# Performance work log

Measured on AMD Instinct MI355X. Metric: run time of the kernel, lower is better.

The kernel has to match this reference:

```python
import jax, jax.numpy as jnp
import numpy as np
from jax import lax

# HF MambaConfig defaults with vocab_size=2048, hidden_size=128
V, DM, NL, I, N, K, R = 2048, 128, 32, 256, 16, 4, 8  # vocab, d_model, layers, intermediate, ssm_state, conv_kernel, dt_rank
B, L = 8, 2048
EPS = 1e-5


def _rms(x, w):
    return x * lax.rsqrt(jnp.mean(x * x, axis=-1, keepdims=True) + EPS) * w


def _block(x, p):
    res = x
    h = _rms(x, p['norm_w'])
    hz = h @ p['in_proj_w'].T                            # (B,L,2I)
    hs, gate = hz[..., :I], hz[..., I:]
    # depthwise causal conv over time
    c = lax.conv_general_dilated(hs.transpose(0, 2, 1), p['conv_w'][:, None, :],
                                 (1,), [(K - 1, 0)],
                                 dimension_numbers=('NCH', 'OIH', 'NCH'),
                                 feature_group_count=I)
    hs = jax.nn.silu((c + p['conv_b'][None, :, None]).transpose(0, 2, 1))  # (B,L,I)
    xp = hs @ p['x_proj_w'].T                            # (B,L,R+2N)
    dt, Bm, Cm = xp[..., :R], xp[..., R:R + N], xp[..., R + N:]
    dt = jax.nn.softplus(dt @ p['dt_proj_w'].T + p['dt_proj_b'])           # (B,L,I)
    A = -jnp.exp(p['A_log'])                             # (I,N)
    dA = jnp.exp(dt[..., None] * A)                      # (B,L,I,N)
    dBu = dt[..., None] * Bm[:, :, None, :] * hs[..., None]               # (B,L,I,N)

    # selective scan: h_t = dA_t * h_{t-1} + dBu_t, via parallel associative scan
    def comb(e1, e2):
        a1, b1 = e1
        a2, b2 = e2
        return a2 * a1, a2 * b1 + b2

    _, hstates = lax.associative_scan(comb, (dA, dBu), axis=1)
    y = jnp.einsum('blin,bln->bli', hstates, Cm) + hs * p['D']
    y = y * jax.nn.silu(gate)
    return res + y @ p['out_proj_w'].T


def setup_inputs() -> dict:
    key = jax.random.key(0)
    ks = jax.random.split(key, 10)

    def rn(k, shape, s):
        return jax.random.normal(k, shape, jnp.float32) * s

    a_init = jnp.tile(jnp.log(jnp.arange(1, N + 1, dtype=jnp.float32)), (NL, I, 1))
    return {
        'x': jax.random.randint(ks[0], (B, L), 0, V),
        'embed': rn(ks[1], (V, DM), 0.02),
        'in_proj_w': rn(ks[2], (NL, 2 * I, DM), DM ** -0.5),
        'conv_w': rn(ks[3], (NL, I, K), K ** -0.5),
        'conv_b': jnp.zeros((NL, I), jnp.float32),
        'x_proj_w': rn(ks[4], (NL, R + 2 * N, I), I ** -0.5),
        'dt_proj_w': rn(ks[5], (NL, I, R), R ** -0.5),
        'dt_proj_b': jnp.full((NL, I), float(np.log(np.expm1(0.01))), jnp.float32),
        'A_log': a_init,
        'D': jnp.ones((NL, I), jnp.float32),
        'out_proj_w': rn(ks[6], (NL, DM, I), I ** -0.5),
        'norm_w': jnp.ones((NL, DM), jnp.float32),
        'norm_f_w': jnp.ones((DM,), jnp.float32),
        'head_w': rn(ks[7], (V, DM), 0.02),
        'head_b': jnp.zeros((V,), jnp.float32),
    }


def reference(x, embed, in_proj_w, conv_w, conv_b, x_proj_w, dt_proj_w, dt_proj_b,
              A_log, D, out_proj_w, norm_w, norm_f_w, head_w, head_b):
    h = embed[x]                                          # (B,L,DM)
    layer_params = {'in_proj_w': in_proj_w, 'conv_w': conv_w, 'conv_b': conv_b,
                    'x_proj_w': x_proj_w, 'dt_proj_w': dt_proj_w, 'dt_proj_b': dt_proj_b,
                    'A_log': A_log, 'D': D, 'out_proj_w': out_proj_w, 'norm_w': norm_w}
    h, _ = lax.scan(lambda c, p: (_block(c, p), None), h, layer_params)
    h = _rms(h, norm_f_w)
    return h @ head_w.T + head_b                          # (B,L,V) logits
```

## Files before the change

kernel.cpp:

```cpp
#include <hip/hip_runtime.h>
#include <hip/hip_bf16.h>

#define LSEQ 2048
#define NCH 64
#define CHL 32

typedef __attribute__((ext_vector_type(8))) short bf16x8;
typedef __attribute__((ext_vector_type(4))) float f32x4;
typedef __hip_bfloat16 bf16;

__device__ __forceinline__ void gload_lds16(const void* g, void* l) {
  __builtin_amdgcn_global_load_lds(
      (const __attribute__((address_space(1))) void*)g,
      (__attribute__((address_space(3))) void*)l, 16, 0, 0);
}

__device__ __forceinline__ void split_bf16(float v, bf16& h, bf16& l) {
  h = __float2bfloat16(v);
  l = __float2bfloat16(v - __bfloat162float(h));
}

__global__ __launch_bounds__(256) void embed_kernel(const int* __restrict__ x,
                                                    const float* __restrict__ emb,
                                                    float* __restrict__ h) {
  int idx = blockIdx.x * 256 + threadIdx.x;
  int t = idx >> 7;
  int d = idx & 127;
  h[idx] = emb[(size_t)x[t] * 128 + d];
}

__global__ __launch_bounds__(256) void cast_split_kernel(const float* __restrict__ src,
                                                         bf16* __restrict__ hi,
                                                         bf16* __restrict__ lo, int n) {
  int i = blockIdx.x * 256 + threadIdx.x;
  if (i < n) { bf16 h, l; split_bf16(src[i], h, l); hi[i] = h; lo[i] = l; }
}

__global__ __launch_bounds__(256) void cast_xproj_kernel(const float* __restrict__ src,
                                                         bf16* __restrict__ hi,
                                                         bf16* __restrict__ lo) {
  int i = blockIdx.x * 256 + threadIdx.x;
  int k = i & 255, n = (i >> 8) & 63, l = i >> 14;
  float v = (n < 40) ? src[((size_t)l * 40 + n) * 256 + k] : 0.f;
  bf16 h, lw; split_bf16(v, h, lw);
  hi[i] = h; lo[i] = lw;
}

__global__ __launch_bounds__(256) void rmsnorm_split_kernel(const float* __restrict__ hin,
                                                            const float* __restrict__ w,
                                                            bf16* __restrict__ hout_h,
                                                            bf16* __restrict__ hout_l) {
  int row = blockIdx.x * 4 + (threadIdx.x >> 6);
  int lane = threadIdx.x & 63;
  float2 v = *(const float2*)&hin[(size_t)row * 128 + lane * 2];
  float ss = v.x * v.x + v.y * v.y;
  #pragma unroll
  for (int m = 1; m < 64; m <<= 1) ss += __shfl_xor(ss, m);
  float rstd = rsqrtf(ss * (1.0f / 128.0f) + 1e-5f);
  float2 wv = *(const float2*)&w[lane * 2];
  float o0 = v.x * rstd * wv.x, o1 = v.y * rstd * wv.y;
  __hip_bfloat162 ph, pl;
  bf16 hh, ll;
  split_bf16(o0, hh, ll); ph.x = hh; pl.x = ll;
  split_bf16(o1, hh, ll); ph.y = hh; pl.y = ll;
  *(__hip_bfloat162*)&hout_h[(size_t)row * 128 + lane * 2] = ph;
  *(__hip_bfloat162*)&hout_l[(size_t)row * 128 + lane * 2] = pl;
}

template <int BM, int BN, int WR, int WC, int EPI>
__global__ __launch_bounds__(256) void mfma_gemm(const bf16* __restrict__ AH,
                                                 const bf16* __restrict__ AL,
                                                 const bf16* __restrict__ WH,
                                                 const bf16* __restrict__ WL,
                                                 float* __restrict__ C,
                                                 const float* __restrict__ bias,
                                                 int Nc, int Kc) {
  constexpr int WTM = BM / WR, WTN = BN / WC;
  constexpr int U = WTM / 16, V = WTN / 16;
  __shared__ bf16 AsH[BM * 64];
  __shared__ bf16 AsL[BM * 64];
  __shared__ bf16 BsH[BN * 64];
  __shared__ bf16 BsL[BN * 64];
  int tid = threadIdx.x;
  int lane = tid & 63, wid = tid >> 6;
  int wr = wid / WC, wc = wid % WC;
  int row0 = blockIdx.x * BM, col0 = blockIdx.y * BN;
  int l15 = lane & 15, l4 = lane >> 4;
  f32x4 acc[U][V] = {};
  for (int k0 = 0; k0 < Kc; k0 += 64) {
    __syncthreads();
    #pragma unroll
    for (int it = 0; it < BM / 32; ++it) {
      int chunk = it * 256 + tid;
      int r = chunk >> 3;
      int clog = (chunk & 7) ^ (r & 7);
      size_t goff = (size_t)(row0 + r) * Kc + k0 + clog * 8;
      gload_lds16(AH + goff, &AsH[chunk * 8]);
      gload_lds16(AL + goff, &AsL[chunk * 8]);
    }
    #pragma unroll
    for (int it = 0; it < BN / 32; ++it) {
      int chunk = it * 256 + tid;
      int r = chunk >> 3;
      int clog = (chunk & 7) ^ (r & 7);
      size_t goff = (size_t)(col0 + r) * Kc + k0 + clog * 8;
      gload_lds16(WH + goff, &BsH[chunk * 8]);
      gload_lds16(WL + goff, &BsL[chunk * 8]);
    }
    __syncthreads();
    #pragma unroll
    for (int kk = 0; kk < 2; ++kk) {
      bf16x8 afh[U], afl[U], bfh[V], bfl[V];
      #pragma unroll
      for (int u = 0; u < U; ++u) {
        int r = wr * WTM + u * 16 + l15;
        int csw = (kk * 4 + l4) ^ (r & 7);
        afh[u] = *(const bf16x8*)&AsH[r * 64 + csw * 8];
        afl[u] = *(const bf16x8*)&AsL[r * 64 + csw * 8];
      }
      #pragma unroll
      for (int v = 0; v < V; ++v) {
        int r = wc * WTN + v * 16 + l15;
        int csw = (kk * 4 + l4) ^ (r & 7);
        bfh[v] = *(const bf16x8*)&BsH[r * 64 + csw * 8];
        bfl[v] = *(const bf16x8*)&BsL[r * 64 + csw * 8];
      }
      #pragma unroll
      for (int u = 0; u < U; ++u)
        #pragma unroll
        for (int v = 0; v < V; ++v) {
          acc[u][v] = __builtin_amdgcn_mfma_f32_16x16x32_bf16(afh[u], bfh[v], acc[u][v], 0, 0, 0);
          acc[u][v] = __builtin_amdgcn_mfma_f32_16x16x32_bf16(afl[u], bfh[v], acc[u][v], 0, 0, 0);
          acc[u][v] = __builtin_amdgcn_mfma_f32_16x16x32_bf16(afh[u], bfl[v], acc[u][v], 0, 0, 0);
        }
    }
  }
  #pragma unroll
  for (int u = 0; u < U; ++u) {
    int rbase = row0 + wr * WTM + u * 16 + l4 * 4;
    #pragma unroll
    for (int v = 0; v < V; ++v) {
      int col = col0 + wc * WTN + v * 16 + l15;
      #pragma unroll
      for (int q = 0; q < 4; ++q) {
        size_t off = (size_t)(rbase + q) * Nc + col;
        float val = acc[u][v][q];
        if (EPI == 2) val += bias[col];
        C[off] = val;
      }
    }
  }
}

__global__ __launch_bounds__(256) void inproj_kernel(const bf16* __restrict__ AH,
                                                     const bf16* __restrict__ AL,
                                                     const bf16* __restrict__ WH,
                                                     const bf16* __restrict__ WL,
                                                     float* __restrict__ hzx,
                                                     float* __restrict__ gate_f) {
  constexpr int BM = 128, BN = 128;
  __shared__ bf16 AsH[BM * 64];
  __shared__ bf16 AsL[BM * 64];
  __shared__ bf16 BsH[BN * 64];
  __shared__ bf16 BsL[BN * 64];
  int tid = threadIdx.x;
  int lane = tid & 63, wid = tid >> 6;
  int wr = wid >> 1, wc = wid & 1;
  int row0 = blockIdx.x * BM, col0 = blockIdx.y * BN;
  int l15 = lane & 15, l4 = lane >> 4;
  f32x4 acc[4][4] = {};
  for (int k0 = 0; k0 < 128; k0 += 64) {
    __syncthreads();
    #pragma unroll
    for (int it = 0; it < 4; ++it) {
      int chunk = it * 256 + tid;
      int r = chunk >> 3;
      int clog = (chunk & 7) ^ (r & 7);
      size_t goff = (size_t)(row0 + r) * 128 + k0 + clog * 8;
      gload_lds16(AH + goff, &AsH[chunk * 8]);
      gload_lds16(AL + goff, &AsL[chunk * 8]);
      size_t woff = (size_t)(col0 + r) * 128 + k0 + clog * 8;
      gload_lds16(WH + woff, &BsH[chunk * 8]);
      gload_lds16(WL + woff, &BsL[chunk * 8]);
    }
    __syncthreads();
    #pragma unroll
    for (int kk = 0; kk < 2; ++kk) {
      bf16x8 afh[4], afl[4], bfh[4], bfl[4];
      #pragma unroll
      for (int u = 0; u < 4; ++u) {
        int r = wr * 64 + u * 16 + l15;
        int csw = (kk * 4 + l4) ^ (r & 7);
        afh[u] = *(const bf16x8*)&AsH[r * 64 + csw * 8];
        afl[u] = *(const bf16x8*)&AsL[r * 64 + csw * 8];
      }
      #pragma unroll
      for (int v = 0; v < 4; ++v) {
        int r = wc * 64 + v * 16 + l15;
        int csw = (kk * 4 + l4) ^ (r & 7);
        bfh[v] = *(const bf16x8*)&BsH[r * 64 + csw * 8];
        bfl[v] = *(const bf16x8*)&BsL[r * 64 + csw * 8];
      }
      #pragma unroll
      for (int u = 0; u < 4; ++u)
        #pragma unroll
        for (int v = 0; v < 4; ++v) {
          acc[u][v] = __builtin_amdgcn_mfma_f32_16x16x32_bf16(afh[u], bfh[v], acc[u][v], 0, 0, 0);
          acc[u][v] = __builtin_amdgcn_mfma_f32_16x16x32_bf16(afl[u], bfh[v], acc[u][v], 0, 0, 0);
          acc[u][v] = __builtin_amdgcn_mfma_f32_16x16x32_bf16(afh[u], bfl[v], acc[u][v], 0, 0, 0);
        }
    }
  }
  bool isgate = (col0 >= 256);
  #pragma unroll
  for (int u = 0; u < 4; ++u) {
    int rbase = row0 + wr * 64 + u * 16 + l4 * 4;
    #pragma unroll
    for (int v = 0; v < 4; ++v) {
      int col = col0 + wc * 64 + v * 16 + l15;
      #pragma unroll
      for (int q = 0; q < 4; ++q) {
        float val = acc[u][v][q];
        if (!isgate) {
          hzx[(size_t)(rbase + q) * 256 + col] = val;
        } else {
          float s = val / (1.0f + __expf(-val));
          gate_f[(size_t)(rbase + q) * 256 + (col - 256)] = s;
        }
      }
    }
  }
}

__global__ __launch_bounds__(256) void xproj_dt_kernel(const float* __restrict__ hzx,
                                                       const float* __restrict__ cw,
                                                       const float* __restrict__ cb,
                                                       const bf16* __restrict__ WH,
                                                       const bf16* __restrict__ WL,
                                                       const float* __restrict__ Wdt,
                                                       const float* __restrict__ bdt,
                                                       __hip_bfloat162* __restrict__ hs_p,
                                                       float* __restrict__ xp,
                                                       float* __restrict__ dtb) {
  __shared__ bf16 AsH[32 * 64];
  __shared__ bf16 AsL[32 * 64];
  __shared__ bf16 BsH[64 * 64];
  __shared__ bf16 BsL[64 * 64];
  __shared__ float xq[32][8];
  int tid = threadIdx.x;
  int lane = tid & 63, wid = tid >> 6;
  int wr = wid >> 1, wc = wid & 1;
  int row0 = blockIdx.x * 32;
  int l15 = lane & 15, l4 = lane >> 4;
  int r = tid >> 3, cslot = tid & 7;
  int tok = row0 + r;
  int lpos = tok & (LSEQ - 1);
  f32x4 acc[1][2] = {};
  for (int k0 = 0; k0 < 256; k0 += 64) {
    __syncthreads();
    {
      int kb = k0 + ((cslot ^ (r & 7)) << 3);
      const float* hp = &hzx[(size_t)tok * 256 + kb];
      float x3[8], x2[8], x1[8], x0[8];
      *(float4*)&x3[0] = *(const float4*)(hp);
      *(float4*)&x3[4] = *(const float4*)(hp + 4);
      if (lpos >= 1) { *(float4*)&x2[0] = *(const float4*)(hp - 256); *(float4*)&x2[4] = *(const float4*)(hp - 252); }
      else { *(float4*)&x2[0] = make_float4(0,0,0,0); *(float4*)&x2[4] = make_float4(0,0,0,0); }
      if (lpos >= 2) { *(float4*)&x1[0] = *(const float4*)(hp - 512); *(float4*)&x1[4] = *(const float4*)(hp - 508); }
      else { *(float4*)&x1[0] = make_float4(0,0,0,0); *(float4*)&x1[4] = make_float4(0,0,0,0); }
      if (lpos >= 3) { *(float4*)&x0[0] = *(const float4*)(hp - 768); *(float4*)&x0[4] = *(const float4*)(hp - 764); }
      else { *(float4*)&x0[0] = make_float4(0,0,0,0); *(float4*)&x0[4] = make_float4(0,0,0,0); }
      bf16 tH[8], tL[8];
      __hip_bfloat162 pk[8];
      #pragma unroll
      for (int j = 0; j < 8; ++j) {
        float4 w = *(const float4*)&cw[(kb + j) * 4];
        float s = cb[kb + j];
        s = fmaf(x0[j], w.x, s);
        s = fmaf(x1[j], w.y, s);
        s = fmaf(x2[j], w.z, s);
        s = fmaf(x3[j], w.w, s);
        s = s / (1.0f + __expf(-s));
        split_bf16(s, tH[j], tL[j]);
        pk[j].x = tH[j]; pk[j].y = tL[j];
      }
      *(bf16x8*)&AsH[tid * 8] = *(const bf16x8*)tH;
      *(bf16x8*)&AsL[tid * 8] = *(const bf16x8*)tL;
      *(float4*)&hs_p[(size_t)tok * 256 + kb]     = *(const float4*)&pk[0];
      *(float4*)&hs_p[(size_t)tok * 256 + kb + 4] = *(const float4*)&pk[4];
    }
    #pragma unroll
    for (int it = 0; it < 2; ++it) {
      int chunk = it * 256 + tid;
      int rr = chunk >> 3;
      int clog = (chunk & 7) ^ (rr & 7);
      size_t goff = (size_t)rr * 256 + k0 + clog * 8;
      gload_lds16(WH + goff, &BsH[chunk * 8]);
      gload_lds16(WL + goff, &BsL[chunk * 8]);
    }
    __syncthreads();
    #pragma unroll
    for (int kk = 0; kk < 2; ++kk) {
      bf16x8 afh, afl, bfh[2], bfl[2];
      {
        int rr = wr * 16 + l15;
        int csw = (kk * 4 + l4) ^ (rr & 7);
        afh = *(const bf16x8*)&AsH[rr * 64 + csw * 8];
        afl = *(const bf16x8*)&AsL[rr * 64 + csw * 8];
      }
      #pragma unroll
      for (int v = 0; v < 2; ++v) {
        int rr = wc * 32 + v * 16 + l15;
        int csw = (kk * 4 + l4) ^ (rr & 7);
        bfh[v] = *(const bf16x8*)&BsH[rr * 64 + csw * 8];
        bfl[v] = *(const bf16x8*)&BsL[rr * 64 + csw * 8];
      }
      #pragma unroll
      for (int v = 0; v < 2; ++v) {
        acc[0][v] = __builtin_amdgcn_mfma_f32_16x16x32_bf16(afh, bfh[v], acc[0][v], 0, 0, 0);
        acc[0][v] = __builtin_amdgcn_mfma_f32_16x16x32_bf16(afl, bfh[v], acc[0][v], 0, 0, 0);
        acc[0][v] = __builtin_amdgcn_mfma_f32_16x16x32_bf16(afh, bfl[v], acc[0][v], 0, 0, 0);
      }
    }
  }
  {
    int rbase = wr * 16 + l4 * 4;
    #pragma unroll
    for (int v = 0; v < 2; ++v) {
      int col = wc * 32 + v * 16 + l15;
      #pragma unroll
      for (int q = 0; q < 4; ++q) {
        float val = acc[0][v][q];
        xp[(size_t)(row0 + rbase + q) * 64 + col] = val;
        if (col < 8) xq[rbase + q][col] = val;
      }
    }
  }
  __syncthreads();
  {
    int i = tid;
    const float* wr8 = Wdt + i * 8;
    float w0 = wr8[0], w1 = wr8[1], w2 = wr8[2], w3 = wr8[3];
    float w4 = wr8[4], w5 = wr8[5], w6 = wr8[6], w7 = wr8[7];
    float bv = bdt[i];
    #pragma unroll 4
    for (int tt = 0; tt < 32; ++tt) {
      const float* q = xq[tt];
      float s = bv;
      s = fmaf(q[0], w0, s); s = fmaf(q[1], w1, s);
      s = fmaf(q[2], w2, s); s = fmaf(q[3], w3, s);
      s = fmaf(q[4], w4, s); s = fmaf(q[5], w5, s);
      s = fmaf(q[6], w6, s); s = fmaf(q[7], w7, s);
      float sp = (s > 20.0f) ? s : log1pf(__expf(s));
      dtb[(size_t)(row0 + tt) * 256 + i] = sp;
    }
  }
}

__global__ __launch_bounds__(256) void outproj_norm_kernel(const bf16* __restrict__ AH,
                                                           const bf16* __restrict__ AL,
                                                           const bf16* __restrict__ WH,
                                                           const bf16* __restrict__ WL,
                                                           const float* __restrict__ nw,
                                                           float* __restrict__ Ch,
                                                           bf16* __restrict__ hn_h,
                                                           bf16* __restrict__ hn_l) {
  constexpr int BM = 32, BN = 128;
  __shared__ bf16 AsH[BM * 64];
  __shared__ bf16 AsL[BM * 64];
  __shared__ bf16 BsH[BN * 64];
  __shared__ bf16 BsL[BN * 64];
  __shared__ float ssq[32][2];
  int tid = threadIdx.x;
  int lane = tid & 63, wid = tid >> 6;
  int wr = wid >> 1, wc = wid & 1;
  int row0 = blockIdx.x * BM;
  int l15 = lane & 15, l4 = lane >> 4;
  f32x4 acc[1][4] = {};
  for (int k0 = 0; k0 < 256; k0 += 64) {
    __syncthreads();
    {
      int chunk = tid;
      int r = chunk >> 3;
      int clog = (chunk & 7) ^ (r & 7);
      size_t goff = (size_t)(row0 + r) * 256 + k0 + clog * 8;
      gload_lds16(AH + goff, &AsH[chunk * 8]);
      gload_lds16(AL + goff, &AsL[chunk * 8]);
    }
    #pragma unroll
    for (int it = 0; it < 4; ++it) {
      int chunk = it * 256 + tid;
      int r = chunk >> 3;
      int clog = (chunk & 7) ^ (r & 7);
      size_t goff = (size_t)r * 256 + k0 + clog * 8;
      gload_lds16(WH + goff, &BsH[chunk * 8]);
      gload_lds16(WL + goff, &BsL[chunk * 8]);
    }
    __syncthreads();
    #pragma unroll
    for (int kk = 0; kk < 2; ++kk) {
      bf16x8 afh, afl, bfh[4], bfl[4];
      {
        int r = wr * 16 + l15;
        int csw = (kk * 4 + l4) ^ (r & 7);
        afh = *(const bf16x8*)&AsH[r * 64 + csw * 8];
        afl = *(const bf16x8*)&AsL[r * 64 + csw * 8];
      }
      #pragma unroll
      for (int v = 0; v < 4; ++v) {
        int r = wc * 64 + v * 16 + l15;
        int csw = (kk * 4 + l4) ^ (r & 7);
        bfh[v] = *(const bf16x8*)&BsH[r * 64 + csw * 8];
        bfl[v] = *(const bf16x8*)&BsL[r * 64 + csw * 8];
      }
      #pragma unroll
      for (int v = 0; v < 4; ++v) {
        acc[0][v] = __builtin_amdgcn_mfma_f32_16x16x32_bf16(afh, bfh[v], acc[0][v], 0, 0, 0);
        acc[0][v] = __builtin_amdgcn_mfma_f32_16x16x32_bf16(afl, bfh[v], acc[0][v], 0, 0, 0);
        acc[0][v] = __builtin_amdgcn_mfma_f32_16x16x32_bf16(afh, bfl[v], acc[0][v], 0, 0, 0);
      }
    }
  }
  int rloc = wr * 16 + l4 * 4;
  float vals[4][4];
  #pragma unroll
  for (int v = 0; v < 4; ++v) {
    int col = wc * 64 + v * 16 + l15;
    #pragma unroll
    for (int q = 0; q < 4; ++q) {
      size_t off = (size_t)(row0 + rloc + q) * 128 + col;
      float val = acc[0][v][q] + Ch[off];
      vals[q][v] = val;
      Ch[off] = val;
    }
  }
  #pragma unroll
  for (int q = 0; q < 4; ++q) {
    float ss = vals[q][0] * vals[q][0] + vals[q][1] * vals[q][1]
             + vals[q][2] * vals[q][2] + vals[q][3] * vals[q][3];
    ss += __shfl_xor(ss, 1, 16);
    ss += __shfl_xor(ss, 2, 16);
    ss += __shfl_xor(ss, 4, 16);
    ss += __shfl_xor(ss, 8, 16);
    if (l15 == 0) ssq[rloc + q][wc] = ss;
  }
  __syncthreads();
  #pragma unroll
  for (int q = 0; q < 4; ++q) {
    float rstd = rsqrtf((ssq[rloc + q][0] + ssq[rloc + q][1]) * (1.0f / 128.0f) + 1e-5f);
    #pragma unroll
    for (int v = 0; v < 4; ++v) {
      int col = wc * 64 + v * 16 + l15;
      float o = vals[q][v] * rstd * nw[col];
      bf16 hh, ll;
      split_bf16(o, hh, ll);
      size_t off = (size_t)(row0 + rloc + q) * 128 + col;
      hn_h[off] = hh;
      hn_l[off] = ll;
    }
  }
}

__global__ __launch_bounds__(256) void scanA_kernel(const float* __restrict__ dtb,
                                                    const __hip_bfloat162* __restrict__ hs_p,
                                                    const float* __restrict__ xp,
                                                    const float* __restrict__ A_log,
                                                    float* __restrict__ Pb,
                                                    float* __restrict__ Sb) {
  int b = blockIdx.x, c = blockIdx.y, i = threadIdx.x;
  float A[16];
  {
    const float4* ap = (const float4*)&A_log[i * 16];
    #pragma unroll
    for (int q = 0; q < 4; ++q) {
      float4 a = ap[q];
      A[q * 4 + 0] = -__expf(a.x); A[q * 4 + 1] = -__expf(a.y);
      A[q * 4 + 2] = -__expf(a.z); A[q * 4 + 3] = -__expf(a.w);
    }
  }
  float P[16], S[16];
  #pragma unroll
  for (int n = 0; n < 16; ++n) { P[n] = 1.0f; S[n] = 0.0f; }
  int t0 = b * LSEQ + c * CHL;
  for (int l = 0; l < CHL; ++l) {
    size_t t = t0 + l;
    float dtv = dtb[t * 256 + i];
    __hip_bfloat162 hp = hs_p[t * 256 + i];
    float hsv = __bfloat162float(hp.x) + __bfloat162float(hp.y);
    float dh = dtv * hsv;
    float Bv[16];
    #pragma unroll
    for (int q = 0; q < 4; ++q) {
      float4 bv = *(const float4*)&xp[t * 64 + 8 + q * 4];
      Bv[q * 4 + 0] = bv.x; Bv[q * 4 + 1] = bv.y; Bv[q * 4 + 2] = bv.z; Bv[q * 4 + 3] = bv.w;
    }
    #pragma unroll
    for (int n = 0; n < 16; ++n) {
      float e = __expf(dtv * A[n]);
      P[n] *= e;
      S[n] = fmaf(S[n], e, dh * Bv[n]);
    }
  }
  size_t base = ((size_t)(b * NCH + c) << 12) + i * 16;
  #pragma unroll
  for (int q = 0; q < 4; ++q) {
    *(float4*)&Pb[base + q * 4] = make_float4(P[q * 4], P[q * 4 + 1], P[q * 4 + 2], P[q * 4 + 3]);
    *(float4*)&Sb[base + q * 4] = make_float4(S[q * 4], S[q * 4 + 1], S[q * 4 + 2], S[q * 4 + 3]);
  }
}

__global__ __launch_bounds__(256) void scanB_kernel(const float* __restrict__ Pb,
                                                    const float* __restrict__ Sb,
                                                    float* __restrict__ Ib) {
  int g = blockIdx.x * 256 + threadIdx.x;
  int b = g >> 12, rem = g & 4095;
  float s = 0.0f;
  for (int cc = 0; cc < NCH; ++cc) {
    size_t off = ((size_t)(b * NCH + cc) << 12) + rem;
    Ib[off] = s;
    s = fmaf(s, Pb[off], Sb[off]);
  }
}

__global__ __launch_bounds__(256) void scanC_kernel(const float* __restrict__ dtb,
                                                    const __hip_bfloat162* __restrict__ hs_p,
                                                    const float* __restrict__ xp,
                                                    const float* __restrict__ A_log,
                                                    const float* __restrict__ Dp,
                                                    const float* __restrict__ gate_f,
                                                    const float* __restrict__ Ib,
                                                    bf16* __restrict__ y_h,
                                                    bf16* __restrict__ y_l) {
  int b = blockIdx.x, c = blockIdx.y, i = threadIdx.x;
  float A[16];
  {
    const float4* ap = (const float4*)&A_log[i * 16];
    #pragma unroll
    for (int q = 0; q < 4; ++q) {
      float4 a = ap[q];
      A[q * 4 + 0] = -__expf(a.x); A[q * 4 + 1] = -__expf(a.y);
      A[q * 4 + 2] = -__expf(a.z); A[q * 4 + 3] = -__expf(a.w);
    }
  }
  float st[16];
  {
    size_t base = ((size_t)(b * NCH + c) << 12) + i * 16;
    #pragma unroll
    for (int q = 0; q < 4; ++q) {
      float4 s4 = *(const float4*)&Ib[base + q * 4];
      st[q * 4 + 0] = s4.x; st[q * 4 + 1] = s4.y; st[q * 4 + 2] = s4.z; st[q * 4 + 3] = s4.w;
    }
  }
  float Dv = Dp[i];
  int t0 = b * LSEQ + c * CHL;
  for (int l = 0; l < CHL; ++l) {
    size_t t = t0 + l;
    float dtv = dtb[t * 256 + i];
    __hip_bfloat162 hp = hs_p[t * 256 + i];
    float hsv = __bfloat162float(hp.x) + __bfloat162float(hp.y);
    float dh = dtv * hsv;
    float Bv[16], Cv[16];
    #pragma unroll
    for (int q = 0; q < 4; ++q) {
      float4 bv = *(const float4*)&xp[t * 64 + 8 + q * 4];
      Bv[q * 4 + 0] = bv.x; Bv[q * 4 + 1] = bv.y; Bv[q * 4 + 2] = bv.z; Bv[q * 4 + 3] = bv.w;
      float4 cv = *(const float4*)&xp[t * 64 + 24 + q * 4];
      Cv[q * 4 + 0] = cv.x; Cv[q * 4 + 1] = cv.y; Cv[q * 4 + 2] = cv.z; Cv[q * 4 + 3] = cv.w;
    }
    float y0 = 0.f, y1 = 0.f, y2 = 0.f, y3 = 0.f;
    #pragma unroll
    for (int q = 0; q < 4; ++q) {
      float e0 = __expf(dtv * A[q * 4 + 0]);
      float e1 = __expf(dtv * A[q * 4 + 1]);
      float e2 = __expf(dtv * A[q * 4 + 2]);
      float e3 = __expf(dtv * A[q * 4 + 3]);
      st[q * 4 + 0] = fmaf(st[q * 4 + 0], e0, dh * Bv[q * 4 + 0]);
      st[q * 4 + 1] = fmaf(st[q * 4 + 1], e1, dh * Bv[q * 4 + 1]);
      st[q * 4 + 2] = fmaf(st[q * 4 + 2], e2, dh * Bv[q * 4 + 2]);
      st[q * 4 + 3] = fmaf(st[q * 4 + 3], e3, dh * Bv[q * 4 + 3]);
      y0 = fmaf(st[q * 4 + 0], Cv[q * 4 + 0], y0);
      y1 = fmaf(st[q * 4 + 1], Cv[q * 4 + 1], y1);
      y2 = fmaf(st[q * 4 + 2], Cv[q * 4 + 2], y2);
      y3 = fmaf(st[q * 4 + 3], Cv[q * 4 + 3], y3);
    }
    float y = ((y0 + y1) + (y2 + y3)) + hsv * Dv;
    float g = gate_f[t * 256 + i];
    float val = y * g;
    bf16 hh, ll;
    split_bf16(val, hh, ll);
    y_h[t * 256 + i] = hh;
    y_l[t * 256 + i] = ll;
  }
}

extern "C" void kernel_launch(void* const* d_in, const int* in_sizes, int n_in,
                              void* d_out, int out_size, void* d_ws, size_t ws_size,
                              hipStream_t stream) {
  const int* x           = (const int*)d_in[0];
  const float* embed     = (const float*)d_in[1];
  const float* in_proj_w = (const float*)d_in[2];
  const float* conv_w    = (const float*)d_in[3];
  const float* conv_b    = (const float*)d_in[4];
  const float* x_proj_w  = (const float*)d_in[5];
  const float* dt_proj_w = (const float*)d_in[6];
  const float* dt_proj_b = (const float*)d_in[7];
  const float* A_log     = (const float*)d_in[8];
  const float* Dp        = (const float*)d_in[9];
  const float* out_proj_w= (const float*)d_in[10];
  const float* norm_w    = (const float*)d_in[11];
  const float* norm_f_w  = (const float*)d_in[12];
  const float* head_w    = (const float*)d_in[13];
  const float* head_b    = (const float*)d_in[14];

  float* out = (float*)d_out;
  float* ws  = (float*)d_ws;

  float* hzx     = out;
  float* Pb      = out;
  float* Sb      = out + 2097152;
  float* gate_f  = out + 4194304;
  __hip_bfloat162* hs_p = (__hip_bfloat162*)(out + 8388608);
  float* dtb     = out + 12582912;
  float* xp      = out + 16777216;
  bf16*  y_h     = (bf16*)(out + 17825792);
  bf16*  y_l     = (bf16*)(out + 19922944);
  float* h       = out + 22020096;
  bf16*  w_in_h  = (bf16*)(out + 24117248);
  bf16*  w_in_l  = (bf16*)(out + 25165824);
  bf16*  w_x_h   = (bf16*)(out + 26214400);
  bf16*  w_x_l   = (bf16*)(out + 26476544);
  bf16*  w_out_h = (bf16*)(out + 26738688);
  bf16*  w_out_l = (bf16*)(out + 27262976);
  float* Ib      = out + 27787264;

  bf16* hn_h     = (bf16*)ws;
  bf16* hn_l     = (bf16*)(ws + 1048576);
  bf16* w_head_h = (bf16*)(ws + 2097152);
  bf16* w_head_l = (bf16*)(ws + 2228224);

  cast_split_kernel<<<8192, 256, 0, stream>>>(in_proj_w, w_in_h, w_in_l, 2097152);
  cast_xproj_kernel<<<2048, 256, 0, stream>>>(x_proj_w, w_x_h, w_x_l);
  cast_split_kernel<<<4096, 256, 0, stream>>>(out_proj_w, w_out_h, w_out_l, 1048576);
  cast_split_kernel<<<1024, 256, 0, stream>>>(head_w, w_head_h, w_head_l, 262144);

  embed_kernel<<<8192, 256, 0, stream>>>(x, embed, h);
  rmsnorm_split_kernel<<<4096, 256, 0, stream>>>(h, norm_w, hn_h, hn_l);

  for (int l = 0; l < 32; ++l) {
    inproj_kernel<<<dim3(128, 4), 256, 0, stream>>>(
        hn_h, hn_l, w_in_h + (size_t)l * 512 * 128, w_in_l + (size_t)l * 512 * 128,
        hzx, gate_f);
    xproj_dt_kernel<<<512, 256, 0, stream>>>(
        hzx, conv_w + l * 1024, conv_b + l * 256,
        w_x_h + (size_t)l * 64 * 256, w_x_l + (size_t)l * 64 * 256,
        dt_proj_w + l * 2048, dt_proj_b + l * 256, hs_p, xp, dtb);
    scanA_kernel<<<dim3(8, NCH), 256, 0, stream>>>(
        dtb, hs_p, xp, A_log + l * 4096, Pb, Sb);
    scanB_kernel<<<128, 256, 0, stream>>>(Pb, Sb, Ib);
    scanC_kernel<<<dim3(8, NCH), 256, 0, stream>>>(
        dtb, hs_p, xp, A_log + l * 4096, Dp + l * 256, gate_f, Ib, y_h, y_l);
    const float* nwnext = (l < 31) ? (norm_w + (l + 1) * 128) : norm_f_w;
    outproj_norm_kernel<<<512, 256, 0, stream>>>(
        y_h, y_l, w_out_h + (size_t)l * 128 * 256, w_out_l + (size_t)l * 128 * 256,
        nwnext, h, hn_h, hn_l);
  }

  mfma_gemm<128, 128, 2, 2, 2><<<dim3(128, 16), 256, 0, stream>>>(
      hn_h, hn_l, w_head_h, w_head_l, out, head_b, 2048, 128);
}
```

Measured before the change: 3.556 ms.

## Fuse chunk-local scan pass into the x_proj/dt kernel

Folds the first pass of the chunked selective scan (per-chunk decay product and partial state) into the x_proj/dt_proj kernel. Each 32-token block is exactly one scan chunk, so dt, hs and B are consumed from registers and LDS instead of being re-read from global memory, and one launch per layer disappears. The Pb/Sb buffers move to the y_h/y_l region because hzx no longer becomes dead before they are written. In exchange the xproj kernel uses more LDS and registers, and its serial 32-step tail now runs 16 exponentials per step, which may lower occupancy.

```diff
diff --git a/kernel.cpp b/kernel.cpp
--- a/kernel.cpp
+++ b/kernel.cpp
@@ -232,21 +232,25 @@
   }
 }
 
-__global__ __launch_bounds__(256) void xproj_dt_kernel(const float* __restrict__ hzx,
-                                                       const float* __restrict__ cw,
-                                                       const float* __restrict__ cb,
-                                                       const bf16* __restrict__ WH,
-                                                       const bf16* __restrict__ WL,
-                                                       const float* __restrict__ Wdt,
-                                                       const float* __restrict__ bdt,
-                                                       __hip_bfloat162* __restrict__ hs_p,
-                                                       float* __restrict__ xp,
-                                                       float* __restrict__ dtb) {
+__global__ __launch_bounds__(256) void xproj_scan_kernel(const float* __restrict__ hzx,
+                                                         const float* __restrict__ cw,
+                                                         const float* __restrict__ cb,
+                                                         const bf16* __restrict__ WH,
+                                                         const bf16* __restrict__ WL,
+                                                         const float* __restrict__ Wdt,
+                                                         const float* __restrict__ bdt,
+                                                         const float* __restrict__ A_log,
+                                                         __hip_bfloat162* __restrict__ hs_p,
+                                                         float* __restrict__ xp,
+                                                         float* __restrict__ dtb,
+                                                         float* __restrict__ Pb,
+                                                         float* __restrict__ Sb) {
   __shared__ bf16 AsH[32 * 64];
   __shared__ bf16 AsL[32 * 64];
   __shared__ bf16 BsH[64 * 64];
   __shared__ bf16 BsL[64 * 64];
-  __shared__ float xq[32][8];
+  __shared__ float xq[32][24];
+  __shared__ __hip_bfloat162 hs_lds[32][257];
   int tid = threadIdx.x;
   int lane = tid & 63, wid = tid >> 6;
   int wr = wid >> 1, wc = wid & 1;
@@ -283,6 +287,7 @@
         s = s / (1.0f + __expf(-s));
         split_bf16(s, tH[j], tL[j]);
         pk[j].x = tH[j]; pk[j].y = tL[j];
+        hs_lds[r][kb + j] = pk[j];
       }
       *(bf16x8*)&AsH[tid * 8] = *(const bf16x8*)tH;
       *(bf16x8*)&AsL[tid * 8] = *(const bf16x8*)tL;
@@ -332,18 +337,30 @@
       for (int q = 0; q < 4; ++q) {
         float val = acc[0][v][q];
         xp[(size_t)(row0 + rbase + q) * 64 + col] = val;
-        if (col < 8) xq[rbase + q][col] = val;
+        if (col < 24) xq[rbase + q][col] = val;
       }
     }
   }
   __syncthreads();
   {
     int i = tid;
+    float A[16];
+    {
+      const float4* ap = (const float4*)&A_log[i * 16];
+      #pragma unroll
+      for (int q = 0; q < 4; ++q) {
+        float4 a = ap[q];
+        A[q * 4 + 0] = -__expf(a.x); A[q * 4 + 1] = -__expf(a.y);
+        A[q * 4 + 2] = -__expf(a.z); A[q * 4 + 3] = -__expf(a.w);
+      }
+    }
     const float* wr8 = Wdt + i * 8;
     float w0 = wr8[0], w1 = wr8[1], w2 = wr8[2], w3 = wr8[3];
     float w4 = wr8[4], w5 = wr8[5], w6 = wr8[6], w7 = wr8[7];
     float bv = bdt[i];
-    #pragma unroll 4
+    float P[16], S[16];
+    #pragma unroll
+    for (int n = 0; n < 16; ++n) { P[n] = 1.0f; S[n] = 0.0f; }
     for (int tt = 0; tt < 32; ++tt) {
       const float* q = xq[tt];
       float s = bv;
@@ -351,8 +368,23 @@
       s = fmaf(q[2], w2, s); s = fmaf(q[3], w3, s);
       s = fmaf(q[4], w4, s); s = fmaf(q[5], w5, s);
       s = fmaf(q[6], w6, s); s = fmaf(q[7], w7, s);
-      float sp = (s > 20.0f) ? s : log1pf(__expf(s));
-      dtb[(size_t)(row0 + tt) * 256 + i] = sp;
+      float dtv = (s > 20.0f) ? s : log1pf(__expf(s));
+      dtb[(size_t)(row0 + tt) * 256 + i] = dtv;
+      __hip_bfloat162 hp = hs_lds[tt][i];
+      float hsv = __bfloat162float(hp.x) + __bfloat162float(hp.y);
+      float dh = dtv * hsv;
+      #pragma unroll
+      for (int n = 0; n < 16; ++n) {
+        float e = __expf(dtv * A[n]);
+        P[n] *= e;
+        S[n] = fmaf(S[n], e, dh * q[8 + n]);
+      }
+    }
+    size_t base = ((size_t)blockIdx.x << 12) + i * 16;
+    #pragma unroll
+    for (int qq = 0; qq < 4; ++qq) {
+      *(float4*)&Pb[base + qq * 4] = make_float4(P[qq * 4], P[qq * 4 + 1], P[qq * 4 + 2], P[qq * 4 + 3]);
+      *(float4*)&Sb[base + qq * 4] = make_float4(S[qq * 4], S[qq * 4 + 1], S[qq * 4 + 2], S[qq * 4 + 3]);
     }
   }
 }
@@ -461,54 +493,6 @@
   }
 }
 
-__global__ __launch_bounds__(256) void scanA_kernel(const float* __restrict__ dtb,
-                                                    const __hip_bfloat162* __restrict__ hs_p,
-                                                    const float* __restrict__ xp,
-                                                    const float* __restrict__ A_log,
-                                                    float* __restrict__ Pb,
-                                                    float* __restrict__ Sb) {
-  int b = blockIdx.x, c = blockIdx.y, i = threadIdx.x;
-  float A[16];
-  {
-    const float4* ap = (const float4*)&A_log[i * 16];
-    #pragma unroll
-    for (int q = 0; q < 4; ++q) {
-      float4 a = ap[q];
-      A[q * 4 + 0] = -__expf(a.x); A[q * 4 + 1] = -__expf(a.y);
-      A[q * 4 + 2] = -__expf(a.z); A[q * 4 + 3] = -__expf(a.w);
-    }
-  }
-  float P[16], S[16];
-  #pragma unroll
-  for (int n = 0; n < 16; ++n) { P[n] = 1.0f; S[n] = 0.0f; }
-  int t0 = b * LSEQ + c * CHL;
-  for (int l = 0; l < CHL; ++l) {
-    size_t t = t0 + l;
-    float dtv = dtb[t * 256 + i];
-    __hip_bfloat162 hp = hs_p[t * 256 + i];
-    float hsv = __bfloat162float(hp.x) + __bfloat162float(hp.y);
-    float dh = dtv * hsv;
-    float Bv[16];
-    #pragma unroll
-    for (int q = 0; q < 4; ++q) {
-      float4 bv = *(const float4*)&xp[t * 64 + 8 + q * 4];
-      Bv[q * 4 + 0] = bv.x; Bv[q * 4 + 1] = bv.y; Bv[q * 4 + 2] = bv.z; Bv[q * 4 + 3] = bv.w;
-    }
-    #pragma unroll
-    for (int n = 0; n < 16; ++n) {
-      float e = __expf(dtv * A[n]);
-      P[n] *= e;
-      S[n] = fmaf(S[n], e, dh * Bv[n]);
-    }
-  }
-  size_t base = ((size_t)(b * NCH + c) << 12) + i * 16;
-  #pragma unroll
-  for (int q = 0; q < 4; ++q) {
-    *(float4*)&Pb[base + q * 4] = make_float4(P[q * 4], P[q * 4 + 1], P[q * 4 + 2], P[q * 4 + 3]);
-    *(float4*)&Sb[base + q * 4] = make_float4(S[q * 4], S[q * 4 + 1], S[q * 4 + 2], S[q * 4 + 3]);
-  }
-}
-
 __global__ __launch_bounds__(256) void scanB_kernel(const float* __restrict__ Pb,
                                                     const float* __restrict__ Sb,
                                                     float* __restrict__ Ib) {
@@ -616,12 +600,12 @@
   float* ws  = (float*)d_ws;
 
   float* hzx     = out;
-  float* Pb      = out;
-  float* Sb      = out + 2097152;
   float* gate_f  = out + 4194304;
   __hip_bfloat162* hs_p = (__hip_bfloat162*)(out + 8388608);
   float* dtb     = out + 12582912;
   float* xp      = out + 16777216;
+  float* Pb      = out + 17825792;
+  float* Sb      = out + 19922944;
   bf16*  y_h     = (bf16*)(out + 17825792);
   bf16*  y_l     = (bf16*)(out + 19922944);
   float* h       = out + 22020096;
@@ -650,12 +634,11 @@
     inproj_kernel<<<dim3(128, 4), 256, 0, stream>>>(
         hn_h, hn_l, w_in_h + (size_t)l * 512 * 128, w_in_l + (size_t)l * 512 * 128,
         hzx, gate_f);
-    xproj_dt_kernel<<<512, 256, 0, stream>>>(
+    xproj_scan_kernel<<<512, 256, 0, stream>>>(
         hzx, conv_w + l * 1024, conv_b + l * 256,
         w_x_h + (size_t)l * 64 * 256, w_x_l + (size_t)l * 64 * 256,
-        dt_proj_w + l * 2048, dt_proj_b + l * 256, hs_p, xp, dtb);
-    scanA_kernel<<<dim3(8, NCH), 256, 0, stream>>>(
-        dtb, hs_p, xp, A_log + l * 4096, Pb, Sb);
+        dt_proj_w + l * 2048, dt_proj_b + l * 256, A_log + l * 4096,
+        hs_p, xp, dtb, Pb, Sb);
     scanB_kernel<<<128, 256, 0, stream>>>(Pb, Sb, Ib);
     scanC_kernel<<<dim3(8, NCH), 256, 0, stream>>>(
         dtb, hs_p, xp, A_log + l * 4096, Dp + l * 256, gate_f, Ib, y_h, y_l);
```

Result: faster. 3.316 ms (-6.8%).
